# Performance work log

Hardware: AMD Instinct MI355X
Metric: run time of the kernel (lower is better)

The kernel has to match this reference:

```python
import jax, jax.numpy as jnp
import numpy as np

MIN_NORM = 1e-15
MARGIN = 9.0
N_ENT, N_REL, DIM = 200000, 500, 64
B, NC = 1024, 1024


def expmap0(u):
    # Poincare ball (c=1) exponential map at origin: tanh(|u|) * u / |u|
    un = jnp.maximum(jnp.linalg.norm(u, axis=-1, keepdims=True), MIN_NORM)
    return jnp.tanh(un) * u / un


def mobius_add(x, y):
    x2 = jnp.sum(x * x, -1, keepdims=True)
    y2 = jnp.sum(y * y, -1, keepdims=True)
    xy = jnp.sum(x * y, -1, keepdims=True)
    num = (1.0 + 2.0 * xy + y2) * x + (1.0 - x2) * y
    den = 1.0 + 2.0 * xy + x2 * y2
    return num / jnp.maximum(den, MIN_NORM)


def givens_rotations(r, x):
    # r, x: [..., D], D even. Rotate consecutive coordinate pairs of x by
    # the normalized 2-vectors of r (cos=g0, sin=g1).
    shp = x.shape
    g = r.reshape(shp[:-1] + (-1, 2))
    g = g / jnp.maximum(jnp.linalg.norm(g, axis=-1, keepdims=True), MIN_NORM)
    xp = x.reshape(shp[:-1] + (-1, 2))
    out = jnp.stack(
        [g[..., 0] * xp[..., 0] - g[..., 1] * xp[..., 1],
         g[..., 1] * xp[..., 0] + g[..., 0] * xp[..., 1]], axis=-1)
    return out.reshape(shp)


def busemann_distance(x, p):
    # B_p(x) = log(|p - x|^2 / (1 - |x|^2)); broadcasts over leading dims
    num = jnp.sum((p - x) ** 2, axis=-1)
    den = 1.0 - jnp.sum(x * x, axis=-1)
    return jnp.log(jnp.maximum(num, MIN_NORM) / jnp.maximum(den, MIN_NORM))


def setup_inputs() -> dict:
    key = jax.random.key(0)
    ks = jax.random.split(key, 9)
    init = 0.001
    return {
        "u_idx": jax.random.randint(ks[0], (B,), 0, N_ENT),
        "r_idx": jax.random.randint(ks[1], (B,), 0, N_REL),
        "v_idx": jax.random.randint(ks[2], (B, NC), 0, N_ENT),
        "emb_entity": init * jax.random.normal(ks[3], (N_ENT, DIM), jnp.float32),
        "rel_diag": 2.0 * jax.random.uniform(ks[4], (N_REL, DIM), jnp.float32) - 1.0,
        "relation_bias_1": init * jax.random.normal(ks[5], (N_REL, DIM), jnp.float32),
        "relation_bias_2": init * jax.random.normal(ks[6], (N_REL, DIM), jnp.float32),
        "bias_head": jnp.zeros((N_ENT,), jnp.float32),
        "bias_tail": jnp.zeros((N_ENT,), jnp.float32),
        "sigma": jax.random.uniform(ks[7], (N_REL,), jnp.float32),
    }


def reference(u_idx, r_idx, v_idx, emb_entity, rel_diag,
              relation_bias_1, relation_bias_2, bias_head, bias_tail, sigma):
    head = expmap0(emb_entity[u_idx])            # [B, D]
    tail = expmap0(emb_entity[v_idx])            # [B, N, D]
    r_b1 = expmap0(relation_bias_1[r_idx])       # [B, D]
    r_b2 = expmap0(relation_bias_2[r_idx])       # [B, D]
    r_d = rel_diag[r_idx]                        # [B, D]

    head = mobius_add(head, r_b1)
    head = givens_rotations(r_d, head)
    head = mobius_add(head, r_b2)                # [B, D]

    head_b = head[:, None, :]                    # broadcast over candidates
    dist_tail = busemann_distance(tail, head_b)  # [B, N]
    dist_head = busemann_distance(head_b, tail)  # [B, N]

    sig = jax.nn.sigmoid(sigma[r_idx])[:, None]  # [B, 1]
    dist = sig * dist_tail + (1.0 - sig) * dist_head
    neg_dist = MARGIN - dist
    return neg_dist + bias_head[u_idx][:, None] + bias_tail[v_idx]
```

## Files before the change

### kernel.cpp

```cpp
#include <hip/hip_runtime.h>

#define MIN_NORM 1e-15f
#define MARGIN 9.0f
#define DIM 64
#define B_ROWS 1024
#define NC 1024

__device__ inline float wave_reduce_sum(float v) {
    #pragma unroll
    for (int off = 32; off > 0; off >>= 1) v += __shfl_xor(v, off, 64);
    return v;
}

__global__ __launch_bounds__(256) void head_kernel(
    const int* __restrict__ u_idx, const int* __restrict__ r_idx,
    const float* __restrict__ emb, const float* __restrict__ rel_diag,
    const float* __restrict__ rb1, const float* __restrict__ rb2,
    const float* __restrict__ bias_head, const float* __restrict__ sigma,
    float* __restrict__ head_out, float* __restrict__ scal_out)
{
    const int lane = threadIdx.x & 63;
    const int row = blockIdx.x * 4 + (threadIdx.x >> 6);
    if (row >= B_ROWS) return;
    const int u = u_idx[row];
    const int r = r_idx[row];

    float x = emb[(long)u * DIM + lane];
    {
        float n2 = wave_reduce_sum(x * x);
        float un = fmaxf(sqrtf(n2), MIN_NORM);
        x = tanhf(un) / un * x;
    }
    float y = rb1[(long)r * DIM + lane];
    {
        float n2 = wave_reduce_sum(y * y);
        float un = fmaxf(sqrtf(n2), MIN_NORM);
        y = tanhf(un) / un * y;
    }
    {
        float x2 = wave_reduce_sum(x * x);
        float y2 = wave_reduce_sum(y * y);
        float xy = wave_reduce_sum(x * y);
        float den = 1.0f + 2.0f * xy + x2 * y2;
        x = ((1.0f + 2.0f * xy + y2) * x + (1.0f - x2) * y) / fmaxf(den, MIN_NORM);
    }
    {
        float g  = rel_diag[(long)r * DIM + lane];
        float go = __shfl_xor(g, 1, 64);
        float xo = __shfl_xor(x, 1, 64);
        float gn = fmaxf(sqrtf(g * g + go * go), MIN_NORM);
        x = ((lane & 1) ? (g * xo + go * x) : (g * x - go * xo)) / gn;
    }
    float z = rb2[(long)r * DIM + lane];
    {
        float n2 = wave_reduce_sum(z * z);
        float un = fmaxf(sqrtf(n2), MIN_NORM);
        z = tanhf(un) / un * z;
    }
    {
        float x2 = wave_reduce_sum(x * x);
        float y2 = wave_reduce_sum(z * z);
        float xy = wave_reduce_sum(x * z);
        float den = 1.0f + 2.0f * xy + x2 * y2;
        x = ((1.0f + 2.0f * xy + y2) * x + (1.0f - x2) * z) / fmaxf(den, MIN_NORM);
    }
    float h2 = wave_reduce_sum(x * x);
    head_out[(long)row * DIM + lane] = x;
    if (lane == 0) {
        scal_out[row * 4 + 0] = h2;
        scal_out[row * 4 + 1] = logf(fmaxf(1.0f - h2, MIN_NORM));
        scal_out[row * 4 + 2] = 1.0f / (1.0f + expf(-sigma[r]));
        scal_out[row * 4 + 3] = bias_head[u];
    }
}

__global__ __launch_bounds__(256) void score_kernel(
    const int* __restrict__ v_idx, const float* __restrict__ emb,
    const float* __restrict__ bias_tail,
    const float* __restrict__ head, const float* __restrict__ scal,
    float* __restrict__ out)
{
    const int b = blockIdx.y;
    const int c = blockIdx.x * 256 + threadIdx.x;

    __shared__ float4 sh[DIM / 4];
    __shared__ float ss[4];
    if (threadIdx.x < DIM / 4)
        sh[threadIdx.x] = ((const float4*)(head + (long)b * DIM))[threadIdx.x];
    if (threadIdx.x < 4)
        ss[threadIdx.x] = scal[b * 4 + threadIdx.x];
    __syncthreads();

    const int v = v_idx[(long)b * NC + c];
    const float4* e4 = (const float4*)(emb + (long)v * DIM);

    float dot = 0.0f, e2 = 0.0f;
    #pragma unroll
    for (int k = 0; k < DIM / 4; ++k) {
        float4 e = e4[k];
        float4 h = sh[k];
        dot = fmaf(h.x, e.x, dot);
        dot = fmaf(h.y, e.y, dot);
        dot = fmaf(h.z, e.z, dot);
        dot = fmaf(h.w, e.w, dot);
        e2 = fmaf(e.x, e.x, e2);
        e2 = fmaf(e.y, e.y, e2);
        e2 = fmaf(e.z, e.z, e2);
        e2 = fmaf(e.w, e.w, e2);
    }

    const float h2 = ss[0], ldh = ss[1], sig = ss[2], bh = ss[3];
    const float un = fmaxf(sqrtf(e2), MIN_NORM);
    const float t = tanhf(un);
    const float s = t / un;
    const float t2 = t * t;
    const float num = h2 + t2 - 2.0f * s * dot;
    const float dist = logf(fmaxf(num, MIN_NORM))
                     - sig * logf(fmaxf(1.0f - t2, MIN_NORM))
                     - (1.0f - sig) * ldh;
    out[(long)b * NC + c] = MARGIN - dist + bh + bias_tail[v];
}

extern "C" void kernel_launch(void* const* d_in, const int* in_sizes, int n_in,
                              void* d_out, int out_size, void* d_ws, size_t ws_size,
                              hipStream_t stream) {
    const int*   u_idx     = (const int*)d_in[0];
    const int*   r_idx     = (const int*)d_in[1];
    const int*   v_idx     = (const int*)d_in[2];
    const float* emb       = (const float*)d_in[3];
    const float* rel_diag  = (const float*)d_in[4];
    const float* rb1       = (const float*)d_in[5];
    const float* rb2       = (const float*)d_in[6];
    const float* bias_head = (const float*)d_in[7];
    const float* bias_tail = (const float*)d_in[8];
    const float* sigma     = (const float*)d_in[9];

    float* head = (float*)d_ws;
    float* scal = head + (long)B_ROWS * DIM;

    head_kernel<<<B_ROWS / 4, 256, 0, stream>>>(
        u_idx, r_idx, emb, rel_diag, rb1, rb2, bias_head, sigma, head, scal);

    score_kernel<<<dim3(NC / 256, B_ROWS), 256, 0, stream>>>(
        v_idx, emb, bias_tail, head, scal, (float*)d_out);
}
```

Measured before the change: 148.8 us.

## Cooperatively gather tail embeddings with four lanes per candidate row

Each group of four threads now loads one int4 of candidate indices and cooperatively reads the four 256-byte embedding rows, each lane taking interleaved float4 chunks. Partial dot products and squared norms are combined with xor shuffles, and each lane then finishes the score for its own candidate. This replaces the old pattern where every thread streamed a whole row alone, which produced strided, poorly coalesced gathers. The cost is extra shuffles and more registers per thread.

```diff
diff --git a/kernel.cpp b/kernel.cpp
--- a/kernel.cpp
+++ b/kernel.cpp
@@ -81,44 +81,74 @@
     float* __restrict__ out)
 {
     const int b = blockIdx.y;
-    const int c = blockIdx.x * 256 + threadIdx.x;
+    const int base = blockIdx.x * 256;
+    const int t = threadIdx.x;
+    const int g = t >> 2;
+    const int sub = t & 3;
 
     __shared__ float4 sh[DIM / 4];
     __shared__ float ss[4];
-    if (threadIdx.x < DIM / 4)
-        sh[threadIdx.x] = ((const float4*)(head + (long)b * DIM))[threadIdx.x];
-    if (threadIdx.x < 4)
-        ss[threadIdx.x] = scal[b * 4 + threadIdx.x];
+    if (t < DIM / 4)
+        sh[t] = ((const float4*)(head + (long)b * DIM))[t];
+    if (t < 4)
+        ss[t] = scal[b * 4 + t];
+
+    const int4 v4 = ((const int4*)(v_idx + (long)b * NC + base))[g];
+    const int v0 = v4.x, v1 = v4.y, v2 = v4.z, v3 = v4.w;
+
     __syncthreads();
 
-    const int v = v_idx[(long)b * NC + c];
-    const float4* e4 = (const float4*)(emb + (long)v * DIM);
+    float4 h[4];
+    #pragma unroll
+    for (int k = 0; k < 4; ++k) h[k] = sh[4 * k + sub];
 
-    float dot = 0.0f, e2 = 0.0f;
-    #pragma unroll
-    for (int k = 0; k < DIM / 4; ++k) {
-        float4 e = e4[k];
-        float4 h = sh[k];
-        dot = fmaf(h.x, e.x, dot);
-        dot = fmaf(h.y, e.y, dot);
-        dot = fmaf(h.z, e.z, dot);
-        dot = fmaf(h.w, e.w, dot);
-        e2 = fmaf(e.x, e.x, e2);
-        e2 = fmaf(e.y, e.y, e2);
-        e2 = fmaf(e.z, e.z, e2);
-        e2 = fmaf(e.w, e.w, e2);
+    float4 e[4][4];
+    {
+        const float4* p0 = (const float4*)(emb + (long)v0 * DIM);
+        const float4* p1 = (const float4*)(emb + (long)v1 * DIM);
+        const float4* p2 = (const float4*)(emb + (long)v2 * DIM);
+        const float4* p3 = (const float4*)(emb + (long)v3 * DIM);
+        #pragma unroll
+        for (int k = 0; k < 4; ++k) {
+            e[0][k] = p0[4 * k + sub];
+            e[1][k] = p1[4 * k + sub];
+            e[2][k] = p2[4 * k + sub];
+            e[3][k] = p3[4 * k + sub];
+        }
     }
 
+    float dot[4], e2[4];
+    #pragma unroll
+    for (int j = 0; j < 4; ++j) {
+        float d = 0.0f, q = 0.0f;
+        #pragma unroll
+        for (int k = 0; k < 4; ++k) {
+            float4 ee = e[j][k];
+            float4 hh = h[k];
+            d = fmaf(hh.x, ee.x, d); d = fmaf(hh.y, ee.y, d);
+            d = fmaf(hh.z, ee.z, d); d = fmaf(hh.w, ee.w, d);
+            q = fmaf(ee.x, ee.x, q); q = fmaf(ee.y, ee.y, q);
+            q = fmaf(ee.z, ee.z, q); q = fmaf(ee.w, ee.w, q);
+        }
+        d += __shfl_xor(d, 1, 64); d += __shfl_xor(d, 2, 64);
+        q += __shfl_xor(q, 1, 64); q += __shfl_xor(q, 2, 64);
+        dot[j] = d; e2[j] = q;
+    }
+
+    const float D  = (sub == 0) ? dot[0] : (sub == 1) ? dot[1] : (sub == 2) ? dot[2] : dot[3];
+    const float E  = (sub == 0) ? e2[0]  : (sub == 1) ? e2[1]  : (sub == 2) ? e2[2]  : e2[3];
+    const int myv  = (sub == 0) ? v0     : (sub == 1) ? v1     : (sub == 2) ? v2     : v3;
+
     const float h2 = ss[0], ldh = ss[1], sig = ss[2], bh = ss[3];
-    const float un = fmaxf(sqrtf(e2), MIN_NORM);
-    const float t = tanhf(un);
-    const float s = t / un;
-    const float t2 = t * t;
-    const float num = h2 + t2 - 2.0f * s * dot;
+    const float un = fmaxf(sqrtf(E), MIN_NORM);
+    const float tn = tanhf(un);
+    const float s = tn / un;
+    const float t2 = tn * tn;
+    const float num = h2 + t2 - 2.0f * s * D;
     const float dist = logf(fmaxf(num, MIN_NORM))
                      - sig * logf(fmaxf(1.0f - t2, MIN_NORM))
                      - (1.0f - sig) * ldh;
-    out[(long)b * NC + c] = MARGIN - dist + bh + bias_tail[v];
+    out[(long)b * NC + base + t] = MARGIN - dist + bh + bias_tail[myv];
 }
 
 extern "C" void kernel_launch(void* const* d_in, const int* in_sizes, int n_in,
```

Result: faster. 139.5 us (-6.3%).
